# Optimization experiments

Hardware: AMD Instinct MI355X
Metric: run time of the kernel (lower is better)

The kernel has to match this reference:

```python
import jax, jax.numpy as jnp
import numpy as np

N, E, D_IN, H = 40000, 640000, 128, 128
R, B = 8, 30  # num_relations = 2*n_speakers**2, num_bases


def setup_inputs() -> dict:
    key = jax.random.key(0)
    ks = jax.random.split(key, 10)
    node_features = jax.random.normal(ks[0], (N, D_IN), jnp.float32)
    edge_index = jax.random.randint(ks[1], (2, E), 0, N)
    edge_type = jax.random.randint(ks[2], (E,), 0, R)
    edge_norm = jax.random.uniform(ks[3], (E,), jnp.float32)
    s_in = 1.0 / np.sqrt(D_IN)
    s_h = 1.0 / np.sqrt(H)
    basis = jax.random.normal(ks[4], (B, D_IN, H), jnp.float32) * s_in
    comp = jax.random.normal(ks[5], (R, B), jnp.float32) * (1.0 / np.sqrt(B))
    root = jax.random.normal(ks[6], (D_IN, H), jnp.float32) * s_in
    bias1 = jnp.zeros((H,), jnp.float32)
    w_rel = jax.random.normal(ks[7], (H, H), jnp.float32) * s_h
    w_root2 = jax.random.normal(ks[8], (H, H), jnp.float32) * s_h
    bias2 = jnp.zeros((H,), jnp.float32)
    return dict(node_features=node_features, edge_index=edge_index,
                edge_norm=edge_norm, edge_type=edge_type,
                basis=basis, comp=comp, root=root, bias1=bias1,
                w_rel=w_rel, w_root2=w_root2, bias2=bias2)


def reference(node_features, edge_index, edge_norm, edge_type,
              basis, comp, root, bias1, w_rel, w_root2, bias2):
    n = node_features.shape[0]
    src, dst = edge_index[0], edge_index[1]  # messages flow src -> dst

    # ---- RGCNConv (basis decomposition, mean aggregation, root + bias) ----
    # Per-relation weights from bases: [R, D_in, H]
    w = jnp.einsum('rb,bio->rio', comp, basis)
    # Transform all nodes by every relation once (avoids per-edge matmul): [R, N, H]
    xw = jnp.einsum('nd,rdo->rno', node_features, w)
    msgs = xw[edge_type, src]                                  # [E, H]
    agg = jax.ops.segment_sum(msgs, dst, num_segments=n)       # [N, H]
    deg = jax.ops.segment_sum(jnp.ones_like(dst, dtype=node_features.dtype),
                              dst, num_segments=n)
    agg = agg / jnp.maximum(deg, 1.0)[:, None]                 # mean aggregation
    h = agg + node_features @ root + bias1                     # [N, H]

    # ---- GraphConv (add aggregation): W_rel * sum_j x_j + W_root * x_i + b ----
    nbr = jax.ops.segment_sum(h[src], dst, num_segments=n)     # [N, H]
    out = nbr @ w_rel + h @ w_root2 + bias2
    return out
```

## Files before the change

### kernel.cpp

```cpp
#include <hip/hip_runtime.h>
#include <stdint.h>

#define DH 128
#define NB 30
#define NR 8

typedef short bf16x8 __attribute__((ext_vector_type(8)));
typedef float f32x4 __attribute__((ext_vector_type(4)));
typedef float f32x2 __attribute__((ext_vector_type(2)));

static __device__ __forceinline__ unsigned short f2bf(float f) {
    unsigned u = __float_as_uint(f);
    u += 0x7fffu + ((u >> 16) & 1u);
    return (unsigned short)(u >> 16);
}
static __device__ __forceinline__ float bflo(unsigned u) { return __uint_as_float(u << 16); }
static __device__ __forceinline__ float bfhi(unsigned u) { return __uint_as_float(u & 0xffff0000u); }

__global__ __launch_bounds__(256) void k_prephist(const float* __restrict__ comp,
                                                  const float* __restrict__ basis,
                                                  const float* __restrict__ root,
                                                  const float* __restrict__ wrel,
                                                  const float* __restrict__ wroot2,
                                                  unsigned short* __restrict__ wallT,
                                                  unsigned short* __restrict__ WT2,
                                                  const int* __restrict__ dstA, int E,
                                                  int* __restrict__ deg, int histB) {
    int b = blockIdx.x;
    int tid = threadIdx.x;
    if (b < histB) {
        int e = b * 256 + tid;
        if (e < E) atomicAdd(&deg[dstA[e]], 1);
        return;
    }
    int unit = (b - histB) * 2 + (tid >> 7);
    int o = tid & 127;
    int i = unit & 127;
    int y = unit >> 7;
    if (y < NR) {
        float s = 0.f;
        #pragma unroll
        for (int bb = 0; bb < NB; ++bb)
            s += comp[y * NB + bb] * basis[((size_t)bb * DH + i) * DH + o];
        wallT[((size_t)y * DH + o) * DH + i] = f2bf(s);
    } else if (y == NR) {
        wallT[((size_t)NR * DH + o) * DH + i] = f2bf(root[i * DH + o]);
    } else {
        const float* W = (y == NR + 2) ? wroot2 : wrel;
        WT2[((size_t)(y - NR - 1) * DH + o) * DH + i] = f2bf(W[i * DH + o]);
    }
}

__global__ __launch_bounds__(1024) void k_scan1(const int* __restrict__ deg, int n, int total_n,
                                                int* __restrict__ offsets, int* __restrict__ partial) {
    __shared__ int s[1024];
    int tid = threadIdx.x;
    int i = blockIdx.x * 1024 + tid;
    int v = (i < n) ? deg[i] : 0;
    s[tid] = v;
    __syncthreads();
    for (int off = 1; off < 1024; off <<= 1) {
        int t = (tid >= off) ? s[tid - off] : 0;
        __syncthreads();
        s[tid] += t;
        __syncthreads();
    }
    if (i < total_n) offsets[i] = s[tid] - v;
    if (tid == 1023) partial[blockIdx.x] = s[1023];
}

__global__ __launch_bounds__(1024) void k_scan3(int* __restrict__ offsets,
                                                const int* __restrict__ partial, int total_n) {
    __shared__ int pre_s;
    if (threadIdx.x == 0) {
        int pre = 0;
        for (int t = 0; t < (int)blockIdx.x; ++t) pre += partial[t];
        pre_s = pre;
    }
    __syncthreads();
    int i = blockIdx.x * 1024 + threadIdx.x;
    if (i < total_n) offsets[i] += pre_s;
}

__global__ void k_scatter(const int* __restrict__ src, const int* __restrict__ dstA,
                          const int* __restrict__ etype, int E,
                          const int* __restrict__ offsets, int* __restrict__ cursor,
                          unsigned* __restrict__ sorted) {
    int e = blockIdx.x * blockDim.x + threadIdx.x;
    if (e >= E) return;
    int d = dstA[e];
    int pos = offsets[d] + atomicAdd(&cursor[d], 1);
    sorted[pos] = (unsigned)src[e] | ((unsigned)etype[e] << 17);
}

__global__ __launch_bounds__(256) void k_gemm1m(const float* __restrict__ x,
                                                const unsigned short* __restrict__ wallT,
                                                const float* __restrict__ bias1,
                                                int Nn,
                                                unsigned* __restrict__ xw8,
                                                unsigned short* __restrict__ hb) {
    __shared__ __align__(16) unsigned short As[128][136];
    __shared__ __align__(16) unsigned short Bs[128][136];
    const int tid = threadIdx.x;
    const int wave = tid >> 6, lane = tid & 63;
    const int g = blockIdx.y;
    const int rowbase = blockIdx.x * 128;
    const int lq = lane >> 4, lr = lane & 15;

    #pragma unroll
    for (int it = 0; it < 8; ++it) {
        int c = it * 256 + tid;
        int row = c >> 4, col = c & 15;
        int rg = rowbase + row; if (rg >= Nn) rg = Nn - 1;
        float4 v0 = *(const float4*)&x[(size_t)rg * DH + col * 8];
        float4 v1 = *(const float4*)&x[(size_t)rg * DH + col * 8 + 4];
        uint4 u;
        u.x = (unsigned)f2bf(v0.x) | ((unsigned)f2bf(v0.y) << 16);
        u.y = (unsigned)f2bf(v0.z) | ((unsigned)f2bf(v0.w) << 16);
        u.z = (unsigned)f2bf(v1.x) | ((unsigned)f2bf(v1.y) << 16);
        u.w = (unsigned)f2bf(v1.z) | ((unsigned)f2bf(v1.w) << 16);
        *(uint4*)&As[row][col * 8] = u;
    }

    for (int rr = 0; rr < 3; ++rr) {
        const int r = g * 3 + rr;
        const unsigned short* WT = wallT + (size_t)r * DH * DH;
        if (rr) __syncthreads();
        #pragma unroll
        for (int it = 0; it < 8; ++it) {
            int c = it * 256 + tid;
            int row = c >> 4, col = c & 15;
            *(uint4*)&Bs[row][col * 8] = *(const uint4*)&WT[(size_t)row * DH + col * 8];
        }
        __syncthreads();

        f32x4 acc[2][8];
        #pragma unroll
        for (int mt = 0; mt < 2; ++mt)
            #pragma unroll
            for (int nt = 0; nt < 8; ++nt) acc[mt][nt] = (f32x4)0.f;

        #pragma unroll
        for (int ks = 0; ks < 4; ++ks) {
            const int ko = ks * 32 + lq * 8;
            bf16x8 a0 = *(const bf16x8*)&As[wave * 32 + lr][ko];
            bf16x8 a1 = *(const bf16x8*)&As[wave * 32 + 16 + lr][ko];
            #pragma unroll
            for (int nt = 0; nt < 8; ++nt) {
                bf16x8 b = *(const bf16x8*)&Bs[nt * 16 + lr][ko];
                acc[0][nt] = __builtin_amdgcn_mfma_f32_16x16x32_bf16(a0, b, acc[0][nt], 0, 0, 0);
                acc[1][nt] = __builtin_amdgcn_mfma_f32_16x16x32_bf16(a1, b, acc[1][nt], 0, 0, 0);
            }
        }
        __syncthreads();

        float bv[8];
        #pragma unroll
        for (int nt = 0; nt < 8; ++nt) bv[nt] = (r == NR) ? bias1[nt * 16 + lr] : 0.f;
        #pragma unroll
        for (int mt = 0; mt < 2; ++mt)
            #pragma unroll
            for (int nt = 0; nt < 8; ++nt)
                #pragma unroll
                for (int reg = 0; reg < 4; ++reg) {
                    int ml = wave * 32 + mt * 16 + lq * 4 + reg;
                    Bs[ml][nt * 16 + lr] = f2bf(acc[mt][nt][reg] + bv[nt]);
                }
        __syncthreads();

        if (r < NR) {
            unsigned* dst = xw8 + ((size_t)r * Nn + rowbase) * (DH / 4);
            #pragma unroll
            for (int it = 0; it < 8; ++it) {
                int c = it * 256 + tid;
                int row = c >> 4, col = c & 15;
                if (rowbase + row < Nn) {
                    uint4 q = *(uint4*)&Bs[row][col * 8];
                    uint2 o;
                    o.x = __builtin_amdgcn_cvt_pk_fp8_f32(bflo(q.x), bfhi(q.x), 0, false);
                    o.x = __builtin_amdgcn_cvt_pk_fp8_f32(bflo(q.y), bfhi(q.y), o.x, true);
                    o.y = __builtin_amdgcn_cvt_pk_fp8_f32(bflo(q.z), bfhi(q.z), 0, false);
                    o.y = __builtin_amdgcn_cvt_pk_fp8_f32(bflo(q.w), bfhi(q.w), o.y, true);
                    *(uint2*)&dst[(size_t)row * (DH / 4) + col * 2] = o;
                }
            }
        } else {
            #pragma unroll
            for (int it = 0; it < 8; ++it) {
                int c = it * 256 + tid;
                int row = c >> 4, col = c & 15;
                if (rowbase + row < Nn)
                    *(uint4*)&hb[((size_t)(rowbase + row)) * DH + col * 8] = *(uint4*)&Bs[row][col * 8];
            }
        }
    }
}

__global__ __launch_bounds__(256) void k_agg1(const int* __restrict__ offsets,
                                              const unsigned* __restrict__ sorted,
                                              const unsigned* __restrict__ xw8,
                                              const unsigned* __restrict__ hb32,
                                              int Nn, unsigned* __restrict__ hbf) {
    int w = (blockIdx.x * blockDim.x + threadIdx.x) >> 6;
    if (w >= Nn) return;
    int lane = threadIdx.x & 63;
    int half = lane >> 5, sub = lane & 31;
    int s = offsets[w], e = offsets[w + 1];
    float a0 = 0.f, a1 = 0.f, a2 = 0.f, a3 = 0.f;
    for (int p = s; p < e; p += 16) {
        unsigned pk[8]; float m[8];
        #pragma unroll
        for (int j = 0; j < 8; ++j) {
            int q = p + 2 * j + half; bool v = q < e;
            pk[j] = sorted[v ? q : e - 1];
            m[j] = v ? 1.f : 0.f;
        }
        unsigned u[8];
        #pragma unroll
        for (int j = 0; j < 8; ++j)
            u[j] = xw8[((size_t)(pk[j] >> 17) * Nn + (pk[j] & 0x1FFFFu)) * 32 + sub];
        #pragma unroll
        for (int j = 0; j < 8; ++j) {
            f32x2 lo = __builtin_amdgcn_cvt_pk_f32_fp8(u[j], false);
            f32x2 hi = __builtin_amdgcn_cvt_pk_f32_fp8(u[j], true);
            a0 = fmaf(m[j], lo.x, a0);
            a1 = fmaf(m[j], lo.y, a1);
            a2 = fmaf(m[j], hi.x, a2);
            a3 = fmaf(m[j], hi.y, a3);
        }
    }
    a0 += __shfl_xor(a0, 32, 64);
    a1 += __shfl_xor(a1, 32, 64);
    a2 += __shfl_xor(a2, 32, 64);
    a3 += __shfl_xor(a3, 32, 64);
    if (half == 0) {
        float invd = 1.0f / fmaxf((float)(e - s), 1.0f);
        uint2 hv = *(const uint2*)&hb32[(size_t)w * 64 + sub * 2];
        float h0 = bflo(hv.x) + a0 * invd;
        float h1 = bfhi(hv.x) + a1 * invd;
        float h2 = bflo(hv.y) + a2 * invd;
        float h3 = bfhi(hv.y) + a3 * invd;
        uint2 o;
        o.x = (unsigned)f2bf(h0) | ((unsigned)f2bf(h1) << 16);
        o.y = (unsigned)f2bf(h2) | ((unsigned)f2bf(h3) << 16);
        *(uint2*)&hbf[(size_t)w * 64 + sub * 2] = o;
    }
}

__global__ __launch_bounds__(256) void k_agg2(const int* __restrict__ offsets,
                                              const unsigned* __restrict__ sorted,
                                              const unsigned* __restrict__ hbf32,
                                              int Nn, unsigned* __restrict__ nbrbf) {
    int w = (blockIdx.x * blockDim.x + threadIdx.x) >> 6;
    if (w >= Nn) return;
    int lane = threadIdx.x & 63;
    int s = offsets[w], e = offsets[w + 1];
    float ax = 0.f, ay = 0.f;
    for (int p = s; p < e; p += 16) {
        unsigned pk[16]; float m[16];
        #pragma unroll
        for (int j = 0; j < 16; ++j) {
            int q = p + j; bool v = q < e;
            pk[j] = sorted[v ? q : e - 1];
            m[j] = v ? 1.f : 0.f;
        }
        unsigned u[16];
        #pragma unroll
        for (int j = 0; j < 16; ++j)
            u[j] = hbf32[(size_t)(pk[j] & 0x1FFFFu) * 64 + lane];
        #pragma unroll
        for (int j = 0; j < 16; ++j) {
            ax = fmaf(m[j], __uint_as_float(u[j] << 16), ax);
            ay = fmaf(m[j], __uint_as_float(u[j] & 0xffff0000u), ay);
        }
    }
    nbrbf[(size_t)w * 64 + lane] = (unsigned)f2bf(ax) | ((unsigned)f2bf(ay) << 16);
}

__global__ __launch_bounds__(256) void k_gemm2m(const unsigned short* __restrict__ nbrbf,
                                                const unsigned short* __restrict__ hbf,
                                                const unsigned short* __restrict__ WT2,
                                                const float* __restrict__ bias2,
                                                int Nn, float* __restrict__ out) {
    __shared__ __align__(16) unsigned short As[128][136];
    __shared__ __align__(16) unsigned short Bs[128][136];
    const int tid = threadIdx.x;
    const int wave = tid >> 6, lane = tid & 63;
    const int rowbase = blockIdx.x * 128;
    const int lq = lane >> 4, lr = lane & 15;

    f32x4 acc[2][8];
    #pragma unroll
    for (int mt = 0; mt < 2; ++mt)
        #pragma unroll
        for (int nt = 0; nt < 8; ++nt) acc[mt][nt] = (f32x4)0.f;

    for (int ph = 0; ph < 2; ++ph) {
        const unsigned short* A = ph ? hbf : nbrbf;
        const unsigned short* WT = WT2 + (size_t)ph * DH * DH;
        if (ph) __syncthreads();
        #pragma unroll
        for (int it = 0; it < 8; ++it) {
            int c = it * 256 + tid;
            int row = c >> 4, col = c & 15;
            int rg = rowbase + row; if (rg >= Nn) rg = Nn - 1;
            *(uint4*)&As[row][col * 8] = *(const uint4*)&A[(size_t)rg * DH + col * 8];
            *(uint4*)&Bs[row][col * 8] = *(const uint4*)&WT[(size_t)row * DH + col * 8];
        }
        __syncthreads();
        #pragma unroll
        for (int ks = 0; ks < 4; ++ks) {
            const int ko = ks * 32 + lq * 8;
            bf16x8 a0 = *(const bf16x8*)&As[wave * 32 + lr][ko];
            bf16x8 a1 = *(const bf16x8*)&As[wave * 32 + 16 + lr][ko];
            #pragma unroll
            for (int nt = 0; nt < 8; ++nt) {
                bf16x8 b = *(const bf16x8*)&Bs[nt * 16 + lr][ko];
                acc[0][nt] = __builtin_amdgcn_mfma_f32_16x16x32_bf16(a0, b, acc[0][nt], 0, 0, 0);
                acc[1][nt] = __builtin_amdgcn_mfma_f32_16x16x32_bf16(a1, b, acc[1][nt], 0, 0, 0);
            }
        }
    }

    float bv[8];
    #pragma unroll
    for (int nt = 0; nt < 8; ++nt) bv[nt] = bias2[nt * 16 + lr];
    #pragma unroll
    for (int mt = 0; mt < 2; ++mt)
        #pragma unroll
        for (int nt = 0; nt < 8; ++nt)
            #pragma unroll
            for (int reg = 0; reg < 4; ++reg) {
                int m = rowbase + wave * 32 + mt * 16 + lq * 4 + reg;
                if (m < Nn) out[(size_t)m * DH + nt * 16 + lr] = acc[mt][nt][reg] + bv[nt];
            }
}

extern "C" void kernel_launch(void* const* d_in, const int* in_sizes, int n_in,
                              void* d_out, int out_size, void* d_ws, size_t ws_size,
                              hipStream_t stream) {
    const float* x      = (const float*)d_in[0];
    const int*   eidx   = (const int*)d_in[1];
    const int*   etype  = (const int*)d_in[3];
    const float* basis  = (const float*)d_in[4];
    const float* comp   = (const float*)d_in[5];
    const float* root   = (const float*)d_in[6];
    const float* bias1  = (const float*)d_in[7];
    const float* wrel   = (const float*)d_in[8];
    const float* wroot2 = (const float*)d_in[9];
    const float* bias2  = (const float*)d_in[10];
    float* out = (float*)d_out;

    const int N = in_sizes[0] / DH;
    const int E = in_sizes[3];
    const int* srcA = eidx;
    const int* dstA = eidx + E;

    char* ws = (char*)d_ws;
    size_t off = 0;
    auto alloc = [&](size_t bytes) -> void* {
        void* p = (void*)(ws + off);
        off += (bytes + 255) & ~(size_t)255;
        return p;
    };
    int* deg           = (int*)alloc((size_t)N * 4);
    int* cursor        = (int*)alloc((size_t)N * 4);
    int* offsets       = (int*)alloc((size_t)(N + 1) * 4);
    int* partial       = (int*)alloc(256 * 4);
    unsigned* sorted   = (unsigned*)alloc((size_t)E * 4);
    unsigned short* wallT = (unsigned short*)alloc((size_t)(NR + 1) * DH * DH * 2);
    unsigned short* WT2   = (unsigned short*)alloc((size_t)2 * DH * DH * 2);
    unsigned* xw8      = (unsigned*)alloc((size_t)NR * N * DH);
    unsigned short* hb = (unsigned short*)alloc((size_t)N * DH * 2);
    unsigned* hbf      = (unsigned*)alloc((size_t)N * (DH / 2) * 4);
    unsigned* nbrbf    = (unsigned*)alloc((size_t)N * (DH / 2) * 4);
    (void)ws_size; (void)n_in; (void)out_size;

    hipMemsetAsync(deg, 0, (size_t)N * 8, stream);

    const int histB = (E + 255) / 256;
    k_prephist<<<histB + 704, 256, 0, stream>>>(comp, basis, root, wrel, wroot2,
                                                wallT, WT2, dstA, E, deg, histB);

    const int totn = N + 1;
    const int nsb = (totn + 1023) / 1024;
    k_scan1<<<nsb, 1024, 0, stream>>>(deg, N, totn, offsets, partial);
    k_scan3<<<nsb, 1024, 0, stream>>>(offsets, partial, totn);
    k_scatter<<<(E + 255) / 256, 256, 0, stream>>>(srcA, dstA, etype, E, offsets, cursor, sorted);

    const int gx = (N + 127) / 128;
    k_gemm1m<<<dim3(gx, 3), 256, 0, stream>>>(x, wallT, bias1, N, xw8, hb);
    k_agg1<<<(N * 64) / 256, 256, 0, stream>>>(offsets, sorted, xw8,
                                               (const unsigned*)hb, N, hbf);
    k_agg2<<<(N * 64) / 256, 256, 0, stream>>>(offsets, sorted, hbf, N, nbrbf);
    k_gemm2m<<<gx, 256, 0, stream>>>((const unsigned short*)nbrbf, (const unsigned short*)hbf,
                                     WT2, bias2, N, out);
}
```

Baseline: 245.2 us.

## Fuse scan passes with decoupled lookback and split agg2 across half-waves

Replaces the two-kernel prefix scan with a single kernel that uses ticket-ordered blocks and decoupled lookback over per-block status words, removing one launch. Both aggregation kernels gain an unmasked fast path for full 16-edge chunks and keep the masked path only for the tail. agg2 now has each half-wave gather 8-byte rows for alternate edges and combines the halves with a cross-lane shuffle, so more gathers are in flight at once. The lookback spin relies on forward progress of earlier blocks, and the memset is enlarged to clear the status words and ticket.

```diff
diff --git a/kernel.cpp b/kernel.cpp
--- a/kernel.cpp
+++ b/kernel.cpp
@@ -51,11 +51,17 @@
     }
 }
 
-__global__ __launch_bounds__(1024) void k_scan1(const int* __restrict__ deg, int n, int total_n,
-                                                int* __restrict__ offsets, int* __restrict__ partial) {
+__global__ __launch_bounds__(1024) void k_scan(const int* __restrict__ deg, int n, int total_n,
+                                               int* __restrict__ offsets,
+                                               unsigned long long* __restrict__ st,
+                                               int* __restrict__ ticket) {
     __shared__ int s[1024];
-    int tid = threadIdx.x;
-    int i = blockIdx.x * 1024 + tid;
+    __shared__ int bid_s, pre_s;
+    const int tid = threadIdx.x;
+    if (tid == 0) bid_s = atomicAdd(ticket, 1);
+    __syncthreads();
+    const int b = bid_s;
+    int i = b * 1024 + tid;
     int v = (i < n) ? deg[i] : 0;
     s[tid] = v;
     __syncthreads();
@@ -65,21 +71,23 @@
         s[tid] += t;
         __syncthreads();
     }
-    if (i < total_n) offsets[i] = s[tid] - v;
-    if (tid == 1023) partial[blockIdx.x] = s[1023];
-}
-
-__global__ __launch_bounds__(1024) void k_scan3(int* __restrict__ offsets,
-                                                const int* __restrict__ partial, int total_n) {
-    __shared__ int pre_s;
-    if (threadIdx.x == 0) {
-        int pre = 0;
-        for (int t = 0; t < (int)blockIdx.x; ++t) pre += partial[t];
-        pre_s = pre;
+    if (tid == 0) {
+        int total = s[1023];
+        atomicExch(&st[b], (1ULL << 62) | (unsigned long long)(unsigned)total);
+        long long pre = 0;
+        int t = b - 1;
+        while (t >= 0) {
+            unsigned long long w;
+            do { w = atomicAdd(&st[t], 0ULL); } while (w == 0ULL);
+            pre += (long long)(w & 0x3FFFFFFFFFFFFFFFULL);
+            if ((w >> 62) == 2ULL) break;
+            --t;
+        }
+        atomicExch(&st[b], (2ULL << 62) | (unsigned long long)(pre + total));
+        pre_s = (int)pre;
     }
     __syncthreads();
-    int i = blockIdx.x * 1024 + threadIdx.x;
-    if (i < total_n) offsets[i] += pre_s;
+    if (i < total_n) offsets[i] = pre_s + s[tid] - v;
 }
 
 __global__ void k_scatter(const int* __restrict__ src, const int* __restrict__ dstA,
@@ -207,7 +215,23 @@
     int half = lane >> 5, sub = lane & 31;
     int s = offsets[w], e = offsets[w + 1];
     float a0 = 0.f, a1 = 0.f, a2 = 0.f, a3 = 0.f;
-    for (int p = s; p < e; p += 16) {
+    int p = s;
+    for (; p + 16 <= e; p += 16) {
+        unsigned pk[8];
+        #pragma unroll
+        for (int j = 0; j < 8; ++j) pk[j] = sorted[p + 2 * j + half];
+        unsigned u[8];
+        #pragma unroll
+        for (int j = 0; j < 8; ++j)
+            u[j] = xw8[((size_t)(pk[j] >> 17) * Nn + (pk[j] & 0x1FFFFu)) * 32 + sub];
+        #pragma unroll
+        for (int j = 0; j < 8; ++j) {
+            f32x2 lo = __builtin_amdgcn_cvt_pk_f32_fp8(u[j], false);
+            f32x2 hi = __builtin_amdgcn_cvt_pk_f32_fp8(u[j], true);
+            a0 += lo.x; a1 += lo.y; a2 += hi.x; a3 += hi.y;
+        }
+    }
+    if (p < e) {
         unsigned pk[8]; float m[8];
         #pragma unroll
         for (int j = 0; j < 8; ++j) {
@@ -249,32 +273,59 @@
 
 __global__ __launch_bounds__(256) void k_agg2(const int* __restrict__ offsets,
                                               const unsigned* __restrict__ sorted,
-                                              const unsigned* __restrict__ hbf32,
-                                              int Nn, unsigned* __restrict__ nbrbf) {
+                                              const uint2* __restrict__ hbf2,
+                                              int Nn, uint2* __restrict__ nbr2) {
     int w = (blockIdx.x * blockDim.x + threadIdx.x) >> 6;
     if (w >= Nn) return;
     int lane = threadIdx.x & 63;
+    int half = lane >> 5, sub = lane & 31;
     int s = offsets[w], e = offsets[w + 1];
-    float ax = 0.f, ay = 0.f;
-    for (int p = s; p < e; p += 16) {
-        unsigned pk[16]; float m[16];
-        #pragma unroll
-        for (int j = 0; j < 16; ++j) {
-            int q = p + j; bool v = q < e;
+    float a0 = 0.f, a1 = 0.f, a2 = 0.f, a3 = 0.f;
+    int p = s;
+    for (; p + 16 <= e; p += 16) {
+        unsigned pk[8];
+        #pragma unroll
+        for (int j = 0; j < 8; ++j) pk[j] = sorted[p + 2 * j + half];
+        uint2 u[8];
+        #pragma unroll
+        for (int j = 0; j < 8; ++j)
+            u[j] = hbf2[(size_t)(pk[j] & 0x1FFFFu) * 32 + sub];
+        #pragma unroll
+        for (int j = 0; j < 8; ++j) {
+            a0 += bflo(u[j].x); a1 += bfhi(u[j].x);
+            a2 += bflo(u[j].y); a3 += bfhi(u[j].y);
+        }
+    }
+    if (p < e) {
+        unsigned pk[8]; float m[8];
+        #pragma unroll
+        for (int j = 0; j < 8; ++j) {
+            int q = p + 2 * j + half; bool v = q < e;
             pk[j] = sorted[v ? q : e - 1];
             m[j] = v ? 1.f : 0.f;
         }
-        unsigned u[16];
-        #pragma unroll
-        for (int j = 0; j < 16; ++j)
-            u[j] = hbf32[(size_t)(pk[j] & 0x1FFFFu) * 64 + lane];
-        #pragma unroll
-        for (int j = 0; j < 16; ++j) {
-            ax = fmaf(m[j], __uint_as_float(u[j] << 16), ax);
-            ay = fmaf(m[j], __uint_as_float(u[j] & 0xffff0000u), ay);
-        }
-    }
-    nbrbf[(size_t)w * 64 + lane] = (unsigned)f2bf(ax) | ((unsigned)f2bf(ay) << 16);
+        uint2 u[8];
+        #pragma unroll
+        for (int j = 0; j < 8; ++j)
+            u[j] = hbf2[(size_t)(pk[j] & 0x1FFFFu) * 32 + sub];
+        #pragma unroll
+        for (int j = 0; j < 8; ++j) {
+            a0 = fmaf(m[j], bflo(u[j].x), a0);
+            a1 = fmaf(m[j], bfhi(u[j].x), a1);
+            a2 = fmaf(m[j], bflo(u[j].y), a2);
+            a3 = fmaf(m[j], bfhi(u[j].y), a3);
+        }
+    }
+    a0 += __shfl_xor(a0, 32, 64);
+    a1 += __shfl_xor(a1, 32, 64);
+    a2 += __shfl_xor(a2, 32, 64);
+    a3 += __shfl_xor(a3, 32, 64);
+    if (half == 0) {
+        uint2 o;
+        o.x = (unsigned)f2bf(a0) | ((unsigned)f2bf(a1) << 16);
+        o.y = (unsigned)f2bf(a2) | ((unsigned)f2bf(a3) << 16);
+        nbr2[(size_t)w * 32 + sub] = o;
+    }
 }
 
 __global__ __launch_bounds__(256) void k_gemm2m(const unsigned short* __restrict__ nbrbf,
@@ -365,8 +416,9 @@
     };
     int* deg           = (int*)alloc((size_t)N * 4);
     int* cursor        = (int*)alloc((size_t)N * 4);
+    unsigned long long* st = (unsigned long long*)alloc(64 * 8);
+    int* ticket        = (int*)alloc(256);
     int* offsets       = (int*)alloc((size_t)(N + 1) * 4);
-    int* partial       = (int*)alloc(256 * 4);
     unsigned* sorted   = (unsigned*)alloc((size_t)E * 4);
     unsigned short* wallT = (unsigned short*)alloc((size_t)(NR + 1) * DH * DH * 2);
     unsigned short* WT2   = (unsigned short*)alloc((size_t)2 * DH * DH * 2);
@@ -376,7 +428,7 @@
     unsigned* nbrbf    = (unsigned*)alloc((size_t)N * (DH / 2) * 4);
     (void)ws_size; (void)n_in; (void)out_size;
 
-    hipMemsetAsync(deg, 0, (size_t)N * 8, stream);
+    hipMemsetAsync(deg, 0, (size_t)N * 8 + 768, stream);
 
     const int histB = (E + 255) / 256;
     k_prephist<<<histB + 704, 256, 0, stream>>>(comp, basis, root, wrel, wroot2,
@@ -384,15 +436,14 @@
 
     const int totn = N + 1;
     const int nsb = (totn + 1023) / 1024;
-    k_scan1<<<nsb, 1024, 0, stream>>>(deg, N, totn, offsets, partial);
-    k_scan3<<<nsb, 1024, 0, stream>>>(offsets, partial, totn);
+    k_scan<<<nsb, 1024, 0, stream>>>(deg, N, totn, offsets, st, ticket);
     k_scatter<<<(E + 255) / 256, 256, 0, stream>>>(srcA, dstA, etype, E, offsets, cursor, sorted);
 
     const int gx = (N + 127) / 128;
     k_gemm1m<<<dim3(gx, 3), 256, 0, stream>>>(x, wallT, bias1, N, xw8, hb);
     k_agg1<<<(N * 64) / 256, 256, 0, stream>>>(offsets, sorted, xw8,
                                                (const unsigned*)hb, N, hbf);
-    k_agg2<<<(N * 64) / 256, 256, 0, stream>>>(offsets, sorted, hbf, N, nbrbf);
+    k_agg2<<<(N * 64) / 256, 256, 0, stream>>>(offsets, sorted, (const uint2*)hbf, N, (uint2*)nbrbf);
     k_gemm2m<<<gx, 256, 0, stream>>>((const unsigned short*)nbrbf, (const unsigned short*)hbf,
                                      WT2, bias2, N, out);
 }
```

After: 243.2 us. No clear change (-0.8%).
